# Optimization experiments

Hardware: AMD Instinct MI355X
Metric: run time of the kernel (lower is better)

## Reference

```python
import jax, jax.numpy as jnp
import numpy as np

ROPE_THETA = 10000.0

def rope(x):
    # RoPE over the FULL model_dim (applied pre head-split, as in the source),
    # interleaved even/odd pairs. x: [B, S, D]
    B, S, D = x.shape
    half = D // 2
    inv_freq = 1.0 / (ROPE_THETA ** (jnp.arange(half, dtype=jnp.float32) * 2.0 / D))
    ang = jnp.arange(S, dtype=jnp.float32)[:, None] * inv_freq[None, :]  # [S, half]
    cos, sin = jnp.cos(ang), jnp.sin(ang)
    x1, x2 = x[..., 0::2], x[..., 1::2]
    r1 = x1 * cos - x2 * sin
    r2 = x1 * sin + x2 * cos
    return jnp.stack([r1, r2], axis=-1).reshape(B, S, D)


def setup_inputs() -> dict:
    key = jax.random.key(0)
    ks = jax.random.split(key, 9)
    B, S, D = 4, 2048, 768
    w = 0.02
    return {
        "X":  jax.random.normal(ks[0], (B, S, D), dtype=jnp.float32),
        "Wq": jax.random.normal(ks[1], (D, D), dtype=jnp.float32) * w,
        "bq": jnp.zeros((D,), dtype=jnp.float32),
        "Wk": jax.random.normal(ks[2], (D, D), dtype=jnp.float32) * w,
        "bk": jnp.zeros((D,), dtype=jnp.float32),
        "Wv": jax.random.normal(ks[3], (D, D), dtype=jnp.float32) * w,
        "bv": jnp.zeros((D,), dtype=jnp.float32),
        "Wo": jax.random.normal(ks[4], (D, D), dtype=jnp.float32) * w,
        "bo": jnp.zeros((D,), dtype=jnp.float32),
    }


def reference(X, Wq, bq, Wk, bk, Wv, bv, Wo, bo):
    NUM_HEADS = 12
    B, S, D = X.shape
    hd = D // NUM_HEADS

    q = rope(X @ Wq + bq)   # RoPE applied pre-split on full model_dim
    k = rope(X @ Wk + bk)
    v = X @ Wv + bv

    # Contiguous per-head slices == reshape to [B, S, H, hd]
    qh = q.reshape(B, S, NUM_HEADS, hd)
    kh = k.reshape(B, S, NUM_HEADS, hd)
    vh = v.reshape(B, S, NUM_HEADS, hd)

    scores = jnp.einsum('bqhd,bkhd->bhqk', qh, kh) / jnp.sqrt(jnp.float32(hd))
    causal = jnp.tril(jnp.ones((S, S), dtype=bool))
    scores = jnp.where(causal[None, None, :, :], scores, -jnp.inf)
    weights = jax.nn.softmax(scores, axis=-1)
    out = jnp.einsum('bhqk,bkhd->bqhd', weights, vh).reshape(B, S, D)
    return out @ Wo + bo
```

## Files before the change

### kernel.cpp

```cpp
#include <hip/hip_runtime.h>
#include <math.h>

#define D_MODEL 768
#define NUM_HEADS 12
#define HEAD_DIM 64
#define SEQ 2048
#define BATCH 4
#define MROWS (BATCH * SEQ)
#define HALF_D (D_MODEL / 2)

typedef __bf16    bf16x8 __attribute__((ext_vector_type(8)));
typedef _Float16  f16x4  __attribute__((ext_vector_type(4)));
typedef float     f32x4  __attribute__((ext_vector_type(4)));

__device__ __forceinline__ void gload_lds16(const void* gp, void* lp) {
    __builtin_amdgcn_global_load_lds(
        (const __attribute__((address_space(1))) unsigned int*)gp,
        (__attribute__((address_space(3))) unsigned int*)lp, 16, 0, 0);
}

__global__ __launch_bounds__(256)
void prep(const float* __restrict__ X, __bf16* __restrict__ Xb,
          const float* __restrict__ W0, const float* __restrict__ W1,
          const float* __restrict__ W2, const float* __restrict__ W3,
          __bf16* __restrict__ T0, __bf16* __restrict__ T1,
          __bf16* __restrict__ T2, __bf16* __restrict__ T3,
          float2* __restrict__ Rt)
{
    __shared__ float t[64][65];
    const int n   = blockIdx.x;
    const int tid = threadIdx.x;

    if (n < 3072) {
        size_t i = ((size_t)n * 256 + tid) * 8;
        float4 u = *(const float4*)(X + i);
        float4 v = *(const float4*)(X + i + 4);
        bf16x8 o;
        o[0]=(__bf16)u.x; o[1]=(__bf16)u.y; o[2]=(__bf16)u.z; o[3]=(__bf16)u.w;
        o[4]=(__bf16)v.x; o[5]=(__bf16)v.y; o[6]=(__bf16)v.z; o[7]=(__bf16)v.w;
        *(bf16x8*)(Xb + i) = o;
    } else if (n < 3648) {
        int m = n - 3072;
        int z = m / 144;
        int rem = m - z * 144;
        int by = rem / 12, bx = rem % 12;
        const float* W = z == 0 ? W0 : z == 1 ? W1 : z == 2 ? W2 : W3;
        __bf16*      T = z == 0 ? T0 : z == 1 ? T1 : z == 2 ? T2 : T3;

        const int r0 = by * 64, c0 = bx * 64;
        const int lx = tid & 63, g = tid >> 6;

        #pragma unroll
        for (int rr = 0; rr < 16; ++rr) {
            int r = g * 16 + rr;
            t[r][lx] = W[(size_t)(r0 + r) * D_MODEL + c0 + lx];
        }
        __syncthreads();

        const int nn = tid >> 2;
        const int kb = (tid & 3) * 16;
        bf16x8 o1, o2;
        #pragma unroll
        for (int mm = 0; mm < 8; ++mm) o1[mm] = (__bf16)t[kb + mm][nn];
        #pragma unroll
        for (int mm = 0; mm < 8; ++mm) o2[mm] = (__bf16)t[kb + 8 + mm][nn];
        __bf16* dst = T + (size_t)(c0 + nn) * D_MODEL + r0 + kb;
        *(bf16x8*)dst       = o1;
        *(bf16x8*)(dst + 8) = o2;
    } else {
        const int m = n - 3648;
        const int e = (m * 256 + tid) * 4;
        const int s  = e / HALF_D;
        const int f0 = e - s * HALF_D;
        const float fs = (float)s;
        float c[4], sv[4];
        #pragma unroll
        for (int u = 0; u < 4; ++u) {
            float fr = __expf((float)(2 * (f0 + u)) * (-9.210340371976184f / 768.0f));
            float ang = fs * fr;
            c[u]  = __cosf(ang);
            sv[u] = __sinf(ang);
        }
        float* dstp = (float*)(Rt + e);
        float4 o01, o23;
        o01.x = c[0]; o01.y = sv[0]; o01.z = c[1]; o01.w = sv[1];
        o23.x = c[2]; o23.y = sv[2]; o23.z = c[3]; o23.w = sv[3];
        *(float4*)dstp       = o01;
        *(float4*)(dstp + 4) = o23;
    }
}

__global__ __launch_bounds__(256)
void qkv_gemm(const __bf16* __restrict__ Xb,
              const __bf16* __restrict__ Wqt, const __bf16* __restrict__ Wkt,
              const __bf16* __restrict__ Wvt,
              const float* __restrict__ bq, const float* __restrict__ bk,
              const float* __restrict__ bv,
              const float2* __restrict__ Rt,
              __bf16* __restrict__ Qb, __bf16* __restrict__ Kb,
              _Float16* __restrict__ Vtb)
{
    __shared__ bf16x8 Asf[2][2][8][64];
    __shared__ bf16x8 Bsf[2][2][8][64];

    const int tid  = threadIdx.x;
    const int wv   = tid >> 6;
    const int ln   = tid & 63;
    const int t15  = ln & 15;
    const int quad = ln >> 4;
    const int wr = wv >> 1, wc = wv & 1;

    const int lin = blockIdx.x;
    const int c   = lin >> 6;
    const int r   = lin & 63;
    const int which = c / 6;
    const int col0  = (c % 6) * 128;
    const int row0  = r * 128;

    const __bf16* Wt  = which == 0 ? Wqt : which == 1 ? Wkt : Wvt;
    const float* bias = which == 0 ? bq  : which == 1 ? bk  : bv;

    f32x4 acc[4][4];
    #pragma unroll
    for (int i = 0; i < 4; ++i)
        #pragma unroll
        for (int j = 0; j < 4; ++j) acc[i][j] = (f32x4){0.f,0.f,0.f,0.f};

    const __bf16* a0 = Xb + (size_t)(row0 + 16 * wv       + t15) * D_MODEL + 8 * quad;
    const __bf16* a1 = Xb + (size_t)(row0 + 16 * (wv + 4) + t15) * D_MODEL + 8 * quad;
    const __bf16* b0 = Wt + (size_t)(col0 + 16 * wv       + t15) * D_MODEL + 8 * quad;
    const __bf16* b1 = Wt + (size_t)(col0 + 16 * (wv + 4) + t15) * D_MODEL + 8 * quad;

    auto stage = [&](int buf, int k0) {
        #pragma unroll
        for (int ks = 0; ks < 2; ++ks) {
            const int kk = k0 + 32 * ks;
            gload_lds16(a0 + kk, &Asf[buf][ks][wv][0]);
            gload_lds16(a1 + kk, &Asf[buf][ks][wv + 4][0]);
            gload_lds16(b0 + kk, &Bsf[buf][ks][wv][0]);
            gload_lds16(b1 + kk, &Bsf[buf][ks][wv + 4][0]);
        }
    };

    stage(0, 0);
    __syncthreads();

    int cur = 0;
    for (int k0 = 0; k0 < D_MODEL; k0 += 64) {
        if (k0 + 64 < D_MODEL)
            stage(cur ^ 1, k0 + 64);

        #pragma unroll
        for (int ks = 0; ks < 2; ++ks) {
            bf16x8 af[4], bfr[4];
            #pragma unroll
            for (int i = 0; i < 4; ++i) af[i]  = Asf[cur][ks][4 * wr + i][ln];
            #pragma unroll
            for (int j = 0; j < 4; ++j) bfr[j] = Bsf[cur][ks][4 * wc + j][ln];
            #pragma unroll
            for (int i = 0; i < 4; ++i)
                #pragma unroll
                for (int j = 0; j < 4; ++j)
                    acc[i][j] = __builtin_amdgcn_mfma_f32_16x16x32_bf16(af[i], bfr[j], acc[i][j], 0, 0, 0);
        }
        __syncthreads();
        cur ^= 1;
    }

    if (which < 2) {
        const float oscale = (which == 0) ? 0.125f : 1.0f;
        __bf16* dst = which ? Kb : Qb;
        #pragma unroll
        for (int i = 0; i < 4; ++i) {
            const int rowb = row0 + 64 * wr + 16 * i + 4 * quad;
            const int s0   = rowb & (SEQ - 1);
            #pragma unroll
            for (int j = 0; j < 4; ++j) {
                const int col = col0 + 64 * wc + 16 * j + t15;
                const float bval = bias[col];
                const float sgn  = (col & 1) ? 1.0f : -1.0f;
                const int   f    = col >> 1;
                #pragma unroll
                for (int rr = 0; rr < 4; ++rr) {
                    float2 cs = Rt[(size_t)(s0 + rr) * HALF_D + f];
                    float val  = acc[i][j][rr] + bval;
                    float part = __shfl_xor(val, 1, 64);
                    dst[(size_t)(rowb + rr) * D_MODEL + col] =
                        (__bf16)((val * cs.x + part * sgn * cs.y) * oscale);
                }
            }
        }
    } else {
        #pragma unroll
        for (int i = 0; i < 4; ++i) {
            const int rowb = row0 + 64 * wr + 16 * i + 4 * quad;
            #pragma unroll
            for (int j = 0; j < 4; ++j) {
                const int col = col0 + 64 * wc + 16 * j + t15;
                const float bval = bias[col];
                const int h = col >> 6, d = col & 63;
                const int bidx = rowb >> 11, s = rowb & (SEQ - 1);
                f16x4 pk;
                #pragma unroll
                for (int rr = 0; rr < 4; ++rr) pk[rr] = (_Float16)(acc[i][j][rr] + bval);
                *(f16x4*)(Vtb + ((size_t)(bidx * NUM_HEADS + h) * 64 + d) * SEQ + s) = pk;
            }
        }
    }
}

__global__ __launch_bounds__(256)
void out_gemm(const __bf16* __restrict__ Ab, const __bf16* __restrict__ Wt,
              const float* __restrict__ bias, float* __restrict__ Cout)
{
    __shared__ bf16x8 Asf[2][2][4][64];
    __shared__ bf16x8 Bsf[2][2][8][64];

    const int tid  = threadIdx.x;
    const int wv   = tid >> 6;
    const int ln   = tid & 63;
    const int t15  = ln & 15;
    const int quad = ln >> 4;
    const int wr = wv >> 1, wc = wv & 1;

    const int lin  = blockIdx.x;
    const int col0 = (lin >> 7) * 128;
    const int row0 = (lin & 127) * 64;

    f32x4 acc[2][4];
    #pragma unroll
    for (int i = 0; i < 2; ++i)
        #pragma unroll
        for (int j = 0; j < 4; ++j) acc[i][j] = (f32x4){0.f,0.f,0.f,0.f};

    auto stage = [&](int buf, int k0) {
        #pragma unroll
        for (int u = 0; u < 6; ++u) {
            const int id = wv * 6 + u;
            const int ks = id / 12;
            const int w  = id % 12;
            if (w < 4) {
                const __bf16* src = Ab + (size_t)(row0 + 16 * w + t15) * D_MODEL
                                       + k0 + 32 * ks + 8 * quad;
                gload_lds16(src, &Asf[buf][ks][w][0]);
            } else {
                const __bf16* src = Wt + (size_t)(col0 + 16 * (w - 4) + t15) * D_MODEL
                                       + k0 + 32 * ks + 8 * quad;
                gload_lds16(src, &Bsf[buf][ks][w - 4][0]);
            }
        }
    };

    stage(0, 0);
    __syncthreads();

    int cur = 0;
    for (int k0 = 0; k0 < D_MODEL; k0 += 64) {
        if (k0 + 64 < D_MODEL)
            stage(cur ^ 1, k0 + 64);

        #pragma unroll
        for (int ks = 0; ks < 2; ++ks) {
            bf16x8 af[2], bfr[4];
            #pragma unroll
            for (int i = 0; i < 2; ++i) af[i]  = Asf[cur][ks][2 * wr + i][ln];
            #pragma unroll
            for (int j = 0; j < 4; ++j) bfr[j] = Bsf[cur][ks][4 * wc + j][ln];
            #pragma unroll
            for (int i = 0; i < 2; ++i)
                #pragma unroll
                for (int j = 0; j < 4; ++j)
                    acc[i][j] = __builtin_amdgcn_mfma_f32_16x16x32_bf16(af[i], bfr[j], acc[i][j], 0, 0, 0);
        }
        __syncthreads();
        cur ^= 1;
    }

    #pragma unroll
    for (int i = 0; i < 2; ++i) {
        const int rowb = row0 + 32 * wr + 16 * i + 4 * quad;
        #pragma unroll
        for (int j = 0; j < 4; ++j) {
            const int col = col0 + 64 * wc + 16 * j + t15;
            const float bval = bias[col];
            #pragma unroll
            for (int rr = 0; rr < 4; ++rr)
                Cout[(size_t)(rowb + rr) * D_MODEL + col] = acc[i][j][rr] + bval;
        }
    }
}

__device__ __forceinline__ void attn_tile(
    const bf16x8 (*Kbuf)[64], const _Float16* Vbuf ,
    bf16x8 aq0, bf16x8 aq1,
    f32x4* o, float& lacc,
    int ln, int t15, int quad, int j0, int qglob, bool domask)
{
    f32x4 s[4];
    #pragma unroll
    for (int c = 0; c < 4; ++c) {
        s[c] = (f32x4){0.f, 0.f, 0.f, 0.f};
        s[c] = __builtin_amdgcn_mfma_f32_16x16x32_bf16(Kbuf[c][ln],     aq0, s[c], 0, 0, 0);
        s[c] = __builtin_amdgcn_mfma_f32_16x16x32_bf16(Kbuf[4 + c][ln], aq1, s[c], 0, 0, 0);
    }

    f16x4 pf[4];
    #pragma unroll
    for (int c = 0; c < 4; ++c)
        #pragma unroll
        for (int r = 0; r < 4; ++r) {
            float e = __expf(s[c][r]);
            if (domask && (j0 + 16 * c + 4 * quad + r > qglob)) e = 0.f;
            lacc += e;
            pf[c][r] = (_Float16)e;
        }

    #pragma unroll
    for (int c = 0; c < 4; ++c) {
        const int lv = 16 * (2 * (c & 1) + (quad >> 1)) + t15;
        const int jb = 4 * (quad & 1);
        #pragma unroll
        for (int cd = 0; cd < 4; ++cd) {
            f16x4 vf = *(const f16x4*)&Vbuf[(size_t)(4 * (c >> 1) + cd) * 512 + lv * 8 + jb];
            o[cd] = __builtin_amdgcn_mfma_f32_16x16x16f16(pf[c], vf, o[cd], 0, 0, 0);
        }
    }
}

__global__ __launch_bounds__(512)
void attn_flash(const __bf16* __restrict__ Q, const __bf16* __restrict__ K,
                const _Float16* __restrict__ Vt, __bf16* __restrict__ O)
{
    __shared__ bf16x8   Kf[2][8][64];
    __shared__ _Float16 Vh[2][8][512];

    const int tid  = threadIdx.x;
    const int wv   = tid >> 6;
    const int ln   = tid & 63;
    const int t15  = ln & 15;
    const int quad = ln >> 4;

    const int n  = blockIdx.x;
    const int qt = 15 - (n / 48);
    const int bh = n % 48;
    const int b  = bh / NUM_HEADS;
    const int h  = bh % NUM_HEADS;
    const int q0 = qt * 128;
    const int nt = (q0 >> 6) + 2;

    bf16x8 aq0, aq1;
    {
        const __bf16* qs = Q + (size_t)(b * SEQ + q0 + 16 * wv + t15) * D_MODEL + h * 64 + 8 * quad;
        aq0 = *(const bf16x8*)qs;
        aq1 = *(const bf16x8*)(qs + 32);
    }

    const __bf16*   kp = K  + ((size_t)b * SEQ + 16 * (wv & 3) + t15) * D_MODEL
                            + h * 64 + 32 * (wv >> 2) + 8 * quad;
    const _Float16* vp = Vt + ((size_t)bh * 64 + 16 * (wv & 3) + t15) * SEQ
                            + 32 * (wv >> 2) + 8 * quad;

    f32x4 o[4];
    #pragma unroll
    for (int c = 0; c < 4; ++c) o[c] = (f32x4){0.f,0.f,0.f,0.f};
    float lacc = 0.f;
    const int qglob = q0 + 16 * wv + t15;
    const int wmax  = q0 + 16 * wv + 15;

    gload_lds16(kp, &Kf[0][wv][0]);
    gload_lds16(vp, &Vh[0][wv][0]);

    int cur = 0;
    for (int it = 0; it < nt; ++it) {
        __syncthreads();
        if (it + 1 < nt) {
            const int jn = (it + 1) * 64;
            gload_lds16(kp + (size_t)jn * D_MODEL, &Kf[cur ^ 1][wv][0]);
            gload_lds16(vp + jn,                   &Vh[cur ^ 1][wv][0]);
        }
        const int j0 = it * 64;
        if (j0 <= wmax) {
            const bool domask = (j0 + 63) > (q0 + 16 * wv);
            attn_tile(Kf[cur], &Vh[cur][0][0], aq0, aq1, o, lacc,
                      ln, t15, quad, j0, qglob, domask);
        }
        cur ^= 1;
    }

    lacc += __shfl_xor(lacc, 16, 64);
    lacc += __shfl_xor(lacc, 32, 64);

    float inv[4];
    #pragma unroll
    for (int r = 0; r < 4; ++r)
        inv[r] = 1.0f / __shfl(lacc, 4 * quad + r, 64);

    #pragma unroll
    for (int c = 0; c < 4; ++c)
        #pragma unroll
        for (int r = 0; r < 4; ++r) {
            int row = q0 + 16 * wv + 4 * quad + r;
            O[(size_t)(b * SEQ + row) * D_MODEL + h * 64 + 16 * c + t15] = (__bf16)(o[c][r] * inv[r]);
        }
}

extern "C" void kernel_launch(void* const* d_in, const int* in_sizes, int n_in,
                              void* d_out, int out_size, void* d_ws, size_t ws_size,
                              hipStream_t stream) {
    const float* X  = (const float*)d_in[0];
    const float* Wq = (const float*)d_in[1];
    const float* bq = (const float*)d_in[2];
    const float* Wk = (const float*)d_in[3];
    const float* bk = (const float*)d_in[4];
    const float* Wv = (const float*)d_in[5];
    const float* bv = (const float*)d_in[6];
    const float* Wo = (const float*)d_in[7];
    const float* bo = (const float*)d_in[8];
    float* out = (float*)d_out;

    const size_t BSD = (size_t)MROWS * D_MODEL;
    const size_t WSZ = (size_t)D_MODEL * D_MODEL;

    __bf16*   Xb  = (__bf16*)d_ws;
    __bf16*   Qb  = Xb  + BSD;
    __bf16*   Kb  = Qb  + BSD;
    _Float16* Vtb = (_Float16*)(Kb + BSD);
    __bf16*   Ob  = (__bf16*)(Vtb + BSD);
    __bf16*   Wqt = Ob  + BSD;
    __bf16*   Wkt = Wqt + WSZ;
    __bf16*   Wvt = Wkt + WSZ;
    __bf16*   Wot = Wvt + WSZ;
    float2*   Rt  = (float2*)(Wot + WSZ);

    prep<<<4416, 256, 0, stream>>>(X, Xb, Wq, Wk, Wv, Wo, Wqt, Wkt, Wvt, Wot, Rt);

    qkv_gemm<<<1152, 256, 0, stream>>>(Xb, Wqt, Wkt, Wvt, bq, bk, bv, Rt, Qb, Kb, Vtb);

    attn_flash<<<768, 512, 0, stream>>>(Qb, Kb, Vtb, Ob);

    out_gemm<<<768, 256, 0, stream>>>(Ob, Wot, bo, out);
}
```

Before: 259.4 us.

## Compute RoPE tables inline and deepen GEMM load pipeline with explicit waitcnt

Removes the precomputed cos/sin table from the prep kernel. The QKV epilogue now computes the rotation angles on the fly, using one sin/cos pair per column and an angle-addition recurrence across the four rows. Both GEMMs now issue two stages of global-to-LDS loads up front and use explicit vmcnt waits with raw barriers, so a load can be in flight while the previous tile is computed. The recurrence changes rounding slightly, and the hand-written waitcnt counts depend on exactly how many loads each stage issues.

```diff
diff --git a/kernel.cpp b/kernel.cpp
--- a/kernel.cpp
+++ b/kernel.cpp
@@ -24,8 +24,7 @@
           const float* __restrict__ W0, const float* __restrict__ W1,
           const float* __restrict__ W2, const float* __restrict__ W3,
           __bf16* __restrict__ T0, __bf16* __restrict__ T1,
-          __bf16* __restrict__ T2, __bf16* __restrict__ T3,
-          float2* __restrict__ Rt)
+          __bf16* __restrict__ T2, __bf16* __restrict__ T3)
 {
     __shared__ float t[64][65];
     const int n   = blockIdx.x;
@@ -39,7 +38,7 @@
         o[0]=(__bf16)u.x; o[1]=(__bf16)u.y; o[2]=(__bf16)u.z; o[3]=(__bf16)u.w;
         o[4]=(__bf16)v.x; o[5]=(__bf16)v.y; o[6]=(__bf16)v.z; o[7]=(__bf16)v.w;
         *(bf16x8*)(Xb + i) = o;
-    } else if (n < 3648) {
+    } else {
         int m = n - 3072;
         int z = m / 144;
         int rem = m - z * 144;
@@ -67,26 +66,6 @@
         __bf16* dst = T + (size_t)(c0 + nn) * D_MODEL + r0 + kb;
         *(bf16x8*)dst       = o1;
         *(bf16x8*)(dst + 8) = o2;
-    } else {
-        const int m = n - 3648;
-        const int e = (m * 256 + tid) * 4;
-        const int s  = e / HALF_D;
-        const int f0 = e - s * HALF_D;
-        const float fs = (float)s;
-        float c[4], sv[4];
-        #pragma unroll
-        for (int u = 0; u < 4; ++u) {
-            float fr = __expf((float)(2 * (f0 + u)) * (-9.210340371976184f / 768.0f));
-            float ang = fs * fr;
-            c[u]  = __cosf(ang);
-            sv[u] = __sinf(ang);
-        }
-        float* dstp = (float*)(Rt + e);
-        float4 o01, o23;
-        o01.x = c[0]; o01.y = sv[0]; o01.z = c[1]; o01.w = sv[1];
-        o23.x = c[2]; o23.y = sv[2]; o23.z = c[3]; o23.w = sv[3];
-        *(float4*)dstp       = o01;
-        *(float4*)(dstp + 4) = o23;
     }
 }
 
@@ -96,7 +75,6 @@
               const __bf16* __restrict__ Wvt,
               const float* __restrict__ bq, const float* __restrict__ bk,
               const float* __restrict__ bv,
-              const float2* __restrict__ Rt,
               __bf16* __restrict__ Qb, __bf16* __restrict__ Kb,
               _Float16* __restrict__ Vtb)
 {
@@ -143,12 +121,17 @@
     };
 
     stage(0, 0);
-    __syncthreads();
-
+    stage(1, 64);
+
+    const int NT = D_MODEL / 64;
     int cur = 0;
-    for (int k0 = 0; k0 < D_MODEL; k0 += 64) {
-        if (k0 + 64 < D_MODEL)
-            stage(cur ^ 1, k0 + 64);
+    for (int t = 0; t < NT; ++t) {
+        if (t < NT - 1) {
+            asm volatile("s_waitcnt vmcnt(8)" ::: "memory");
+        } else {
+            asm volatile("s_waitcnt vmcnt(0)" ::: "memory");
+        }
+        __builtin_amdgcn_s_barrier();
 
         #pragma unroll
         for (int ks = 0; ks < 2; ++ks) {
@@ -163,7 +146,10 @@
                 for (int j = 0; j < 4; ++j)
                     acc[i][j] = __builtin_amdgcn_mfma_f32_16x16x32_bf16(af[i], bfr[j], acc[i][j], 0, 0, 0);
         }
-        __syncthreads();
+
+        asm volatile("s_waitcnt lgkmcnt(0)" ::: "memory");
+        __builtin_amdgcn_s_barrier();
+        if (t + 2 < NT) stage(cur, 64 * (t + 2));
         cur ^= 1;
     }
 
@@ -178,15 +164,21 @@
             for (int j = 0; j < 4; ++j) {
                 const int col = col0 + 64 * wc + 16 * j + t15;
                 const float bval = bias[col];
-                const float sgn  = (col & 1) ? 1.0f : -1.0f;
-                const int   f    = col >> 1;
+                const int ne = col & ~1;
+                const float fr = __expf((float)ne * (-9.210340371976184f / 768.0f));
+                const float cf = __cosf(fr), sf = __sinf(fr);
+                const float sgn = (col & 1) ? 1.0f : -1.0f;
+                float ang = (float)s0 * fr;
+                float ca = __cosf(ang), sa = __sinf(ang);
                 #pragma unroll
                 for (int rr = 0; rr < 4; ++rr) {
-                    float2 cs = Rt[(size_t)(s0 + rr) * HALF_D + f];
+                    const int rw = rowb + rr;
                     float val  = acc[i][j][rr] + bval;
                     float part = __shfl_xor(val, 1, 64);
-                    dst[(size_t)(rowb + rr) * D_MODEL + col] =
-                        (__bf16)((val * cs.x + part * sgn * cs.y) * oscale);
+                    dst[(size_t)rw * D_MODEL + col] = (__bf16)((val * ca + part * sgn * sa) * oscale);
+                    float cn = ca * cf - sa * sf;
+                    sa = sa * cf + ca * sf;
+                    ca = cn;
                 }
             }
         }
@@ -252,12 +244,17 @@
     };
 
     stage(0, 0);
-    __syncthreads();
-
+    stage(1, 64);
+
+    const int NT = D_MODEL / 64;
     int cur = 0;
-    for (int k0 = 0; k0 < D_MODEL; k0 += 64) {
-        if (k0 + 64 < D_MODEL)
-            stage(cur ^ 1, k0 + 64);
+    for (int t = 0; t < NT; ++t) {
+        if (t < NT - 1) {
+            asm volatile("s_waitcnt vmcnt(6)" ::: "memory");
+        } else {
+            asm volatile("s_waitcnt vmcnt(0)" ::: "memory");
+        }
+        __builtin_amdgcn_s_barrier();
 
         #pragma unroll
         for (int ks = 0; ks < 2; ++ks) {
@@ -272,7 +269,10 @@
                 for (int j = 0; j < 4; ++j)
                     acc[i][j] = __builtin_amdgcn_mfma_f32_16x16x32_bf16(af[i], bfr[j], acc[i][j], 0, 0, 0);
         }
-        __syncthreads();
+
+        asm volatile("s_waitcnt lgkmcnt(0)" ::: "memory");
+        __builtin_amdgcn_s_barrier();
+        if (t + 2 < NT) stage(cur, 64 * (t + 2));
         cur ^= 1;
     }
 
@@ -430,11 +430,10 @@
     __bf16*   Wkt = Wqt + WSZ;
     __bf16*   Wvt = Wkt + WSZ;
     __bf16*   Wot = Wvt + WSZ;
-    float2*   Rt  = (float2*)(Wot + WSZ);
-
-    prep<<<4416, 256, 0, stream>>>(X, Xb, Wq, Wk, Wv, Wo, Wqt, Wkt, Wvt, Wot, Rt);
-
-    qkv_gemm<<<1152, 256, 0, stream>>>(Xb, Wqt, Wkt, Wvt, bq, bk, bv, Rt, Qb, Kb, Vtb);
+
+    prep<<<3648, 256, 0, stream>>>(X, Xb, Wq, Wk, Wv, Wo, Wqt, Wkt, Wvt, Wot);
+
+    qkv_gemm<<<1152, 256, 0, stream>>>(Xb, Wqt, Wkt, Wvt, bq, bk, bv, Qb, Kb, Vtb);
 
     attn_flash<<<768, 512, 0, stream>>>(Qb, Kb, Vtb, Ob);
 
```

Result: faster. 242.3 us (-6.6%).
